# Performance work log

Measured on AMD Instinct MI355X. Metric: run time of the kernel, lower is better.

Reference implementation:

```python
import jax, jax.numpy as jnp
import numpy as np

EMBED_DIM = 2048
NUM_HEADS = 16
HEAD_DIM = EMBED_DIM // NUM_HEADS
ROPE_BASE = 10000.0


def _rope_cos_sin(seq_len, head_dim, dtype):
    # half-split (LLaMA-style) rotary embedding tables, shape [S, D]
    inv_freq = 1.0 / (ROPE_BASE ** (jnp.arange(0, head_dim, 2, dtype=jnp.float32) / head_dim))
    ang = jnp.arange(seq_len, dtype=jnp.float32)[:, None] * inv_freq[None, :]  # [S, D/2]
    cos = jnp.concatenate([jnp.cos(ang), jnp.cos(ang)], axis=-1).astype(dtype)
    sin = jnp.concatenate([jnp.sin(ang), jnp.sin(ang)], axis=-1).astype(dtype)
    return cos, sin


def _rotate_half(t):
    d = t.shape[-1] // 2
    return jnp.concatenate([-t[..., d:], t[..., :d]], axis=-1)


def setup_inputs() -> dict:
    key = jax.random.key(0)
    ks = jax.random.split(key, 9)
    B, S, E = 2, 2048, EMBED_DIM
    sc = 1.0 / np.sqrt(E)
    return {
        "x": jax.random.normal(ks[0], (B, S, E), jnp.float32),
        "Wq": jax.random.normal(ks[1], (E, E), jnp.float32) * sc,
        "bq": jax.random.normal(ks[2], (E,), jnp.float32) * 0.01,
        "Wk": jax.random.normal(ks[3], (E, E), jnp.float32) * sc,
        "bk": jax.random.normal(ks[4], (E,), jnp.float32) * 0.01,
        "Wv": jax.random.normal(ks[5], (E, E), jnp.float32) * sc,
        "bv": jax.random.normal(ks[6], (E,), jnp.float32) * 0.01,
        "Wo": jax.random.normal(ks[7], (E, E), jnp.float32) * sc,
        "bo": jax.random.normal(ks[8], (E,), jnp.float32) * 0.01,
    }


def reference(x, Wq, bq, Wk, bk, Wv, bv, Wo, bo):
    B, S, E = x.shape
    H, D = NUM_HEADS, HEAD_DIM

    def split_heads(t):  # [B,S,E] -> [B,H,S,D]
        return t.reshape(B, S, H, D).transpose(0, 2, 1, 3)

    # torch nn.Linear: y = x @ W^T + b
    q = split_heads(x @ Wq.T + bq)
    k = split_heads(x @ Wk.T + bk)
    v = split_heads(x @ Wv.T + bv)

    cos, sin = _rope_cos_sin(S, D, x.dtype)  # [S, D]
    q = q * cos + _rotate_half(q) * sin
    k = k * cos + _rotate_half(k) * sin

    scale = 1.0 / jnp.sqrt(jnp.asarray(D, x.dtype))
    scores = jnp.einsum("bhsd,bhtd->bhst", q, k) * scale  # [B,H,S,S]
    attn = jax.nn.softmax(scores, axis=-1)
    ctx = jnp.einsum("bhst,bhtd->bhsd", attn, v)  # [B,H,S,D]
    ctx = ctx.transpose(0, 2, 1, 3).reshape(B, S, E)
    return ctx @ Wo.T + bo
```

## Files before the change

kernel.cpp:

```cpp
#include <hip/hip_runtime.h>
#include <stdint.h>

typedef unsigned short u16;
typedef unsigned int u32;
typedef __bf16 bf16x8 __attribute__((ext_vector_type(8)));
typedef u16 u16x8 __attribute__((ext_vector_type(8)));
typedef float f32x4 __attribute__((ext_vector_type(4)));
typedef float f32x16 __attribute__((ext_vector_type(16)));

#define NB 2
#define NS 2048
#define NE 2048
#define NH 16
#define ND 128
#define NM (NB*NS)

__device__ __forceinline__ float bf2f(u16 u){
  union { unsigned u; float f; } v; v.u = ((unsigned)u) << 16; return v.f;
}
__device__ __forceinline__ u16 f2bf(float f){
  union { float f; unsigned u; } v; v.f = f;
  unsigned r = v.u + 0x7fffu + ((v.u >> 16) & 1u);
  return (u16)(r >> 16);
}
__device__ __forceinline__ void gl_lds16(const u16* g, u16* l){
  __builtin_amdgcn_global_load_lds((const __attribute__((address_space(1))) unsigned int*)g,
                                   (__attribute__((address_space(3))) unsigned int*)l, 16, 0, 0);
}

__global__ __launch_bounds__(256) void k_prep(const float* __restrict__ x,
                                              const float* __restrict__ w0, const float* __restrict__ w1,
                                              const float* __restrict__ w2, const float* __restrict__ w3,
                                              u16* __restrict__ xo,
                                              u16* __restrict__ o0, u16* __restrict__ o1,
                                              u16* __restrict__ o2, u16* __restrict__ o3,
                                              float* __restrict__ cosT, float* __restrict__ sinT){
  const int NX = NM * NE / 4;
  const int NW = NE * NE / 4;
  const int NC = NX + 4 * NW;
  const int NT = NS * 64;
  const int TOT = NC + NT;
  for (int i = blockIdx.x * 256 + threadIdx.x; i < TOT; i += gridDim.x * 256){
    if (i < NC){
      const float* in; u16* out; int off;
      if (i < NX){ in = x; out = xo; off = i; }
      else {
        int j = i - NX; int sg = j >> 20; off = j & (NW - 1);
        in  = sg == 0 ? w0 : sg == 1 ? w1 : sg == 2 ? w2 : w3;
        out = sg == 0 ? o0 : sg == 1 ? o1 : sg == 2 ? o2 : o3;
      }
      float4 v = ((const float4*)in)[off];
      ushort4 o;
      o.x = f2bf(v.x); o.y = f2bf(v.y); o.z = f2bf(v.z); o.w = f2bf(v.w);
      ((ushort4*)out)[off] = o;
    } else {
      int idx = i - NC;
      int s = idx >> 6, ii = idx & 63;
      float inv = exp2f(-(float)(2 * ii) * (13.287712379549449f / 128.0f));
      float ang = (float)s * inv;
      float c = cosf(ang), sn = sinf(ang);
      cosT[s * ND + ii]      = c;  cosT[s * ND + 64 + ii] = c;
      sinT[s * ND + ii]      = sn; sinT[s * ND + 64 + ii] = sn;
    }
  }
}

template<int MODE>
__global__ __launch_bounds__(512, 2) void k_gemm(const u16* __restrict__ A, const u16* __restrict__ W,
                                                 const float* __restrict__ bias,
                                                 const float* __restrict__ cosT, const float* __restrict__ sinT,
                                                 float qs, void* __restrict__ outp)
{
  __shared__ __align__(16) u16 lds[49152];
  const int t    = threadIdx.x;
  const int lane = t & 63;
  const int g    = lane >> 4;
  const int q    = lane & 15;
  const int wid  = t >> 6;
  const int wr   = (wid >> 1) * 64;
  const int wc   = (wid & 1) * 64;

  const int bid = blockIdx.x;
  const int v   = (bid & 7) * 32 + (bid >> 3);
  const int bm  = (v >> 4) * 256;
  const int bn  = (v & 15) * 128;

  int aoff[4], aldso[4], boff[2], bldso[2];
  #pragma unroll
  for (int c = 0; c < 4; ++c){
    int o = c * 8192 + t * 16;
    int row = o >> 7;
    int cb = (o & 127) ^ ((row & 7) << 4);
    aldso[c] = o >> 1;
    aoff[c]  = row * NE + (cb >> 1);
  }
  #pragma unroll
  for (int c = 0; c < 2; ++c){
    int o = c * 8192 + t * 16;
    int row = o >> 7;
    int cb = (o & 127) ^ ((row & 7) << 4);
    bldso[c] = o >> 1;
    boff[c]  = row * NE + (cb >> 1);
  }
  const u16* Abase = A + (size_t)bm * NE;
  const u16* Wbase = W + (size_t)bn * NE;

  int ard[2][4], brd[2][4];
  #pragma unroll
  for (int kk = 0; kk < 2; ++kk){
    #pragma unroll
    for (int m = 0; m < 4; ++m){
      int row = wr + m * 16 + q;
      ard[kk][m] = row * 128 + ((kk * 64 + g * 16) ^ ((row & 7) << 4));
    }
    #pragma unroll
    for (int n = 0; n < 4; ++n){
      int row = wc + n * 16 + q;
      brd[kk][n] = row * 128 + ((kk * 64 + g * 16) ^ ((row & 7) << 4));
    }
  }

  #pragma unroll
  for (int c = 0; c < 4; ++c) gl_lds16(Abase + aoff[c], lds + aldso[c]);
  #pragma unroll
  for (int c = 0; c < 2; ++c) gl_lds16(Wbase + boff[c], lds + 16384 + bldso[c]);

  f32x4 acc[4][4] = {};

  for (int kt = 0; kt < 32; ++kt){
    const int cbb = (kt & 1) ? 24576 : 0;
    if (kt < 31){
      const int sbb = cbb ^ 24576;
      const int go  = (kt + 1) * 64;
      #pragma unroll
      for (int c = 0; c < 4; ++c) gl_lds16(Abase + go + aoff[c], lds + sbb + aldso[c]);
      #pragma unroll
      for (int c = 0; c < 2; ++c) gl_lds16(Wbase + go + boff[c], lds + sbb + 16384 + bldso[c]);
      asm volatile("s_waitcnt vmcnt(6)" ::: "memory");
    } else {
      asm volatile("s_waitcnt vmcnt(0)" ::: "memory");
    }
    __builtin_amdgcn_s_barrier();

    const char* Ap = (const char*)(lds + cbb);
    const char* Bp = (const char*)(lds + cbb + 16384);

    #pragma unroll
    for (int kk = 0; kk < 2; ++kk){
      bf16x8 af[4], bfr[4];
      #pragma unroll
      for (int m = 0; m < 4; ++m) af[m]  = *(const bf16x8*)(Ap + ard[kk][m]);
      #pragma unroll
      for (int n = 0; n < 4; ++n) bfr[n] = *(const bf16x8*)(Bp + brd[kk][n]);
      __builtin_amdgcn_s_setprio(1);
      #pragma unroll
      for (int m = 0; m < 4; ++m)
        #pragma unroll
        for (int n = 0; n < 4; ++n)
          acc[m][n] = __builtin_amdgcn_mfma_f32_16x16x32_bf16(af[m], bfr[n], acc[m][n], 0, 0, 0);
      __builtin_amdgcn_s_setprio(0);
    }
    __builtin_amdgcn_s_barrier();
  }

  if constexpr (MODE == 2){
    float* out = (float*)outp;
    #pragma unroll
    for (int m = 0; m < 4; ++m)
      #pragma unroll
      for (int n = 0; n < 4; ++n){
        int col = bn + wc + n * 16 + q;
        float bv = bias[col];
        #pragma unroll
        for (int j = 0; j < 4; ++j){
          int row = bm + wr + m * 16 + g * 4 + j;
          out[(size_t)row * NE + col] = acc[m][n][j] + bv;
        }
      }
  } else if constexpr (MODE == 1){
    u16* out = (u16*)outp;
    __syncthreads();
    #pragma unroll
    for (int m = 0; m < 4; ++m)
      #pragma unroll
      for (int n = 0; n < 4; ++n){
        int d = wc + n * 16 + q;
        float bv = bias[bn + d];
        #pragma unroll
        for (int j = 0; j < 4; ++j){
          int sl = wr + m * 16 + g * 4 + j;
          lds[d * 264 + sl] = f2bf(acc[m][n][j] + bv);
        }
      }
    __syncthreads();
    const int b = bm >> 11, h = bn >> 7, sbase = bm & 2047;
    const int dq = t >> 4;
    const int sq = (t & 15) * 16;
    #pragma unroll
    for (int rep = 0; rep < 4; ++rep){
      int d = rep * 32 + dq;
      const u16* src = lds + d * 264 + sq;
      u16* dp = out + ((size_t)((b * NH + h) * ND + d)) * NS + sbase + sq;
      *(u16x8*)(dp)     = *(const u16x8*)(src);
      *(u16x8*)(dp + 8) = *(const u16x8*)(src + 8);
    }
  } else {
    u16* out = (u16*)outp;
    __syncthreads();
    #pragma unroll
    for (int m = 0; m < 4; ++m)
      #pragma unroll
      for (int n = 0; n < 4; ++n){
        int cl = wc + n * 16 + q;
        float bv = bias[bn + cl];
        #pragma unroll
        for (int j = 0; j < 4; ++j){
          int rl = wr + m * 16 + g * 4 + j;
          lds[rl * 132 + cl] = f2bf(acc[m][n][j] + bv);
        }
      }
    __syncthreads();
    #pragma unroll
    for (int m = 0; m < 4; ++m)
      #pragma unroll
      for (int n = 0; n < 4; ++n){
        int cl  = wc + n * 16 + q;
        int col = bn + cl;
        int h = col >> 7;
        float bv = bias[col];
        #pragma unroll
        for (int j = 0; j < 4; ++j){
          int rl = wr + m * 16 + g * 4 + j;
          int row = bm + rl;
          int b = row >> 11, s = row & 2047;
          float mine    = acc[m][n][j] + bv;
          float partner = bf2f(lds[rl * 132 + (cl ^ 64)]);
          float rot = (cl < 64) ? -partner : partner;
          float val = (mine * cosT[s * ND + cl] + rot * sinT[s * ND + cl]) * qs;
          out[(((size_t)(b * NH + h)) * NS + s) * ND + cl] = f2bf(val);
        }
      }
  }
}

template<bool D1>
__device__ __forceinline__ void pswap(u32 &a, u32 &b){
  if constexpr (D1) asm volatile("v_permlane32_swap_b32 %0, %1" : "+v"(a), "+v"(b));
  else              asm volatile("v_permlane32_swap_b32 %0, %1" : "+v"(b), "+v"(a));
}

#define AT_BODY(KT, SCC, SCN, KSTG, VSTG, KNXT, VCUR, SK, SV, VM, LAST)               \
  {                                                                                   \
    if (SK){ const int kb = ((KT) + 2) * 64 * ND;                                     \
      _Pragma("unroll") for (int c = 0; c < 4; ++c)                                   \
        gl_lds16(Kbase + kb + koff[c], (KSTG) + kldso[c]); }                          \
    if (SV){ const int vb = ((KT) + 1) * 64;                                          \
      _Pragma("unroll") for (int c = 0; c < 4; ++c)                                   \
        gl_lds16(Vbase + vb + voff[c], (VSTG) + vldso[c]); }                          \
    asm volatile("s_waitcnt vmcnt(" VM ")" ::: "memory");                             \
    __builtin_amdgcn_s_barrier();                                                     \
    float ts = 0.f;                                                                   \
    if (!(LAST)){                                                                     \
      SCN[0] = (f32x16)(0.f);                                                         \
      __builtin_amdgcn_s_setprio(1);                                                  \
      _Pragma("unroll") for (int kk = 0; kk < 8; ++kk){                               \
        bf16x8 kf = *(const bf16x8*)((KNXT) + krd[0][kk]);                            \
        SCN[0] = __builtin_amdgcn_mfma_f32_32x32x16_bf16(kf, qf[kk], SCN[0], 0, 0, 0);\
      }                                                                               \
      __builtin_amdgcn_s_setprio(0);                                                  \
    }                                                                                 \
    _Pragma("unroll") for (int r = 0; r < 16; ++r){                                   \
      float e = exp2f(SCC[0][r]); SCC[0][r] = e; ts += e; }                           \
    if (!(LAST)){                                                                     \
      SCN[1] = (f32x16)(0.f);                                                         \
      __builtin_amdgcn_s_setprio(1);                                                  \
      _Pragma("unroll") for (int kk = 0; kk < 8; ++kk){                               \
        bf16x8 kf = *(const bf16x8*)((KNXT) + krd[1][kk]);                            \
        SCN[1] = __builtin_amdgcn_mfma_f32_32x32x16_bf16(kf, qf[kk], SCN[1], 0, 0, 0);\
      }                                                                               \
      __builtin_amdgcn_s_setprio(0);                                                  \
    }                                                                                 \
    _Pragma("unroll") for (int r = 0; r < 16; ++r){                                   \
      float e = exp2f(SCC[1][r]); SCC[1][r] = e; ts += e; }                           \
    ts += __shfl_xor(ts, 32);                                                         \
    lrow += ts;                                                                       \
    __builtin_amdgcn_s_setprio(1);                                                    \
    _Pragma("unroll") for (int t2 = 0; t2 < 2; ++t2)                                  \
      _Pragma("unroll") for (int kk2 = 0; kk2 < 2; ++kk2){                            \
        u32 a0, a1, b0, b1;                                                           \
        asm("v_cvt_pk_bf16_f32 %0, %1, %2" : "=v"(a0) : "v"(SCC[t2][8*kk2+0]), "v"(SCC[t2][8*kk2+1])); \
        asm("v_cvt_pk_bf16_f32 %0, %1, %2" : "=v"(a1) : "v"(SCC[t2][8*kk2+2]), "v"(SCC[t2][8*kk2+3])); \
        asm("v_cvt_pk_bf16_f32 %0, %1, %2" : "=v"(b0) : "v"(SCC[t2][8*kk2+4]), "v"(SCC[t2][8*kk2+5])); \
        asm("v_cvt_pk_bf16_f32 %0, %1, %2" : "=v"(b1) : "v"(SCC[t2][8*kk2+6]), "v"(SCC[t2][8*kk2+7])); \
        pswap<D1>(a0, b0); pswap<D1>(a1, b1);                                         \
        union { u32 u[4]; bf16x8 v; } pf;                                             \
        pf.u[0] = a0; pf.u[1] = a1; pf.u[2] = b0; pf.u[3] = b1;                       \
        const int kkf = 2*t2 + kk2;                                                   \
        _Pragma("unroll") for (int dt = 0; dt < 4; ++dt){                             \
          bf16x8 vf = *(const bf16x8*)((VCUR) + vrd[kkf][dt]);                        \
          acc[dt] = __builtin_amdgcn_mfma_f32_32x32x16_bf16(vf, pf.v, acc[dt], 0, 0, 0); \
        }                                                                             \
      }                                                                               \
    __builtin_amdgcn_s_setprio(0);                                                    \
    if (!(LAST)) __builtin_amdgcn_s_barrier();                                        \
  }

template<bool D1>
__device__ __forceinline__ void attn_impl(const u16* __restrict__ Qa, const u16* __restrict__ Ka,
                                          const u16* __restrict__ Vt, u16* __restrict__ ctx,
                                          u16* Ks0, u16* Ks1, u16* Vs0, u16* Vs1)
{
  const int t    = threadIdx.x;
  const int lane = t & 63;
  const int w    = t >> 6;
  const int l31  = lane & 31;
  const int hi   = lane >> 5;

  const int v   = (blockIdx.x & 7) * 64 + (blockIdx.x >> 3);
  const int qb  = v & 15;
  const int bh  = v >> 4;
  const int q0  = qb * 128 + w * 32;

  int koff[4], kldso[4], voff[4], vldso[4];
  #pragma unroll
  for (int c = 0; c < 4; ++c){
    int o = c * 4096 + t * 16;
    { int row = o >> 8, col = o & 255; int cs = col ^ ((row & 15) << 4);
      kldso[c] = o >> 1;  koff[c] = row * ND + (cs >> 1); }
    { int row = o >> 7, col = o & 127; int cs = col ^ ((row & 7) << 4);
      vldso[c] = o >> 1;  voff[c] = row * NS + (cs >> 1); }
  }
  const u16* Kbase = Ka + (size_t)bh * NS * ND;
  const u16* Vbase = Vt + (size_t)bh * ND * NS;

  bf16x8 qf[8];
  #pragma unroll
  for (int kk = 0; kk < 8; ++kk)
    qf[kk] = *(const bf16x8*)(Qa + ((size_t)bh * NS + q0 + l31) * ND + kk * 16 + hi * 8);

  #pragma unroll
  for (int c = 0; c < 4; ++c) gl_lds16(Kbase + koff[c], Ks0 + kldso[c]);
  #pragma unroll
  for (int c = 0; c < 4; ++c) gl_lds16(Vbase + voff[c], Vs0 + vldso[c]);
  #pragma unroll
  for (int c = 0; c < 4; ++c) gl_lds16(Kbase + 64 * ND + koff[c], Ks1 + kldso[c]);

  int krd[2][8], vrd[4][4];
  #pragma unroll
  for (int t2 = 0; t2 < 2; ++t2){
    const int row = t2 * 32 + l31, sw = (row & 15) << 4;
    #pragma unroll
    for (int kk = 0; kk < 8; ++kk)
      krd[t2][kk] = row * 256 + ((kk * 32 + hi * 16) ^ sw);
  }
  #pragma unroll
  for (int dt = 0; dt < 4; ++dt){
    const int row = dt * 32 + l31, sw = (row & 7) << 4;
    #pragma unroll
    for (int kk = 0; kk < 4; ++kk)
      vrd[kk][dt] = row * 128 + ((kk * 32 + hi * 16) ^ sw);
  }

  asm volatile("s_waitcnt vmcnt(8)" ::: "memory");
  __builtin_amdgcn_s_barrier();

  f32x16 scA[2], scB[2];
  scA[0] = (f32x16)(0.f); scA[1] = (f32x16)(0.f);
  {
    const char* Kl = (const char*)Ks0;
    #pragma unroll
    for (int t2 = 0; t2 < 2; ++t2)
      #pragma unroll
      for (int kk = 0; kk < 8; ++kk){
        bf16x8 kf = *(const bf16x8*)(Kl + krd[t2][kk]);
        scA[t2] = __builtin_amdgcn_mfma_f32_32x32x16_bf16(kf, qf[kk], scA[t2], 0, 0, 0);
      }
  }
  __builtin_amdgcn_s_barrier();

  f32x16 acc[4] = {};
  float lrow = 0.f;

  for (int kt = 0; kt < 30; kt += 2){
    AT_BODY(kt,     scA, scB, Ks0, Vs1, (const char*)Ks1, (const char*)Vs0, 1, 1, "8", 0);
    AT_BODY(kt + 1, scB, scA, Ks1, Vs0, (const char*)Ks0, (const char*)Vs1, 1, 1, "8", 0);
  }
  AT_BODY(30, scA, scB, Ks0, Vs1, (const char*)Ks1, (const char*)Vs0, 0, 1, "4", 0);
  AT_BODY(31, scB, scA, Ks1, Vs0, (const char*)Ks0, (const char*)Vs1, 0, 0, "0", 1);

  const float inv = 1.0f / lrow;
  const int b = bh >> 4, h = bh & 15;
  const int s = q0 + l31;
  #pragma unroll
  for (int dt = 0; dt < 4; ++dt)
    #pragma unroll
    for (int a2 = 0; a2 < 4; ++a2){
      const int d0 = dt * 32 + 8 * a2 + 4 * hi;
      ushort4 o;
      o.x = f2bf(acc[dt][4*a2+0] * inv);
      o.y = f2bf(acc[dt][4*a2+1] * inv);
      o.z = f2bf(acc[dt][4*a2+2] * inv);
      o.w = f2bf(acc[dt][4*a2+3] * inv);
      *(ushort4*)(ctx + ((size_t)(b * NS + s)) * NE + h * ND + d0) = o;
    }
}

__global__ __launch_bounds__(256, 2) void k_attn(const u16* __restrict__ Qa, const u16* __restrict__ Ka,
                                                 const u16* __restrict__ Vt, u16* __restrict__ ctx)
{
  __shared__ __align__(16) u16 Ks[2][64 * 128];
  __shared__ __align__(16) u16 Vs[2][128 * 64];
  const int lane = threadIdx.x & 63;
  u32 xx = (u32)lane, yy = 64u + (u32)lane;
  asm volatile("v_permlane32_swap_b32 %0, %1" : "+v"(xx), "+v"(yy));
  const bool isD1 = (xx == (u32)(lane < 32 ? lane : lane + 32));
  if (isD1) attn_impl<true >(Qa, Ka, Vt, ctx, &Ks[0][0], &Ks[1][0], &Vs[0][0], &Vs[1][0]);
  else      attn_impl<false>(Qa, Ka, Vt, ctx, &Ks[0][0], &Ks[1][0], &Vs[0][0], &Vs[1][0]);
}

extern "C" void kernel_launch(void* const* d_in, const int* in_sizes, int n_in,
                              void* d_out, int out_size, void* d_ws, size_t ws_size,
                              hipStream_t stream)
{
  const float* x  = (const float*)d_in[0];
  const float* Wq = (const float*)d_in[1];
  const float* bq = (const float*)d_in[2];
  const float* Wk = (const float*)d_in[3];
  const float* bk = (const float*)d_in[4];
  const float* Wv = (const float*)d_in[5];
  const float* bv = (const float*)d_in[6];
  const float* Wo = (const float*)d_in[7];
  const float* bo = (const float*)d_in[8];

  char* ws = (char*)d_ws;
  u16*   xbf  = (u16*)(ws);
  u16*   wqb  = (u16*)(ws + 16777216);
  u16*   wkb  = (u16*)(ws + 25165824);
  u16*   wvb  = (u16*)(ws + 33554432);
  u16*   wob  = (u16*)(ws + 41943040);
  float* cosT = (float*)(ws + 50331648);
  float* sinT = (float*)(ws + 51380224);
  u16*   Qa   = (u16*)(ws + 52428800);
  u16*   Ka   = (u16*)(ws + 69206016);
  u16*   Vt   = (u16*)(ws + 85983232);
  u16*   ctx  = xbf;

  const float sl = 0.08838834764831845f * 1.4426950408889634f;

  k_prep<<<2048, 256, 0, stream>>>(x, Wq, Wk, Wv, Wo, xbf, wqb, wkb, wvb, wob, cosT, sinT);

  k_gemm<0><<<256, 512, 0, stream>>>(xbf, wqb, bq, cosT, sinT, sl,   (void*)Qa);
  k_gemm<0><<<256, 512, 0, stream>>>(xbf, wkb, bk, cosT, sinT, 1.0f, (void*)Ka);
  k_gemm<1><<<256, 512, 0, stream>>>(xbf, wvb, bv, nullptr, nullptr, 1.0f, (void*)Vt);

  k_attn<<<512, 256, 0, stream>>>(Qa, Ka, Vt, ctx);

  k_gemm<2><<<256, 512, 0, stream>>>(ctx, wob, bo, nullptr, nullptr, 1.0f, d_out);
}
```

Measured before the change: 269.7 us.

## Fuse Q/K/V projections into one GEMM launch with triple-buffered LDS

Replaces the three separate Q, K and V projection GEMM launches with one 768-block kernel over a concatenated weight (wqb, wkb, wvb assumed contiguous), picking the epilogue per column segment. The K-loop moves from double to triple buffering of LDS (73728 u16 = 144 KB), which drops the trailing barrier per iteration. The attention row-sum cross-lane shuffle is hoisted out of the inner loop to a single final shuffle. Risks: 144 KB LDS per block limits residency to one block per CU despite launch_bounds(512,2), and removing the end-of-iteration barrier relies on the third buffer to avoid overwrite races.

```diff
diff --git a/kernel.cpp b/kernel.cpp
--- a/kernel.cpp
+++ b/kernel.cpp
@@ -65,154 +65,133 @@
   }
 }
 
-template<int MODE>
-__global__ __launch_bounds__(512, 2) void k_gemm(const u16* __restrict__ A, const u16* __restrict__ W,
-                                                 const float* __restrict__ bias,
-                                                 const float* __restrict__ cosT, const float* __restrict__ sinT,
-                                                 float qs, void* __restrict__ outp)
+#define GEMM_PREAMBLE                                                                 \
+  const int t    = threadIdx.x;                                                      \
+  const int lane = t & 63;                                                           \
+  const int g    = lane >> 4;                                                        \
+  const int q    = lane & 15;                                                        \
+  const int wid  = t >> 6;                                                           \
+  const int wr   = (wid >> 1) * 64;                                                  \
+  const int wc   = (wid & 1) * 64;                                                   \
+  int aoff[4], aldso[4], boff[2], bldso[2];                                          \
+  _Pragma("unroll") for (int c = 0; c < 4; ++c){                                     \
+    int o = c * 8192 + t * 16;                                                       \
+    int row = o >> 7;                                                                \
+    int cb2 = (o & 127) ^ ((row & 7) << 4);                                          \
+    aldso[c] = o >> 1;                                                               \
+    aoff[c]  = row * NE + (cb2 >> 1);                                                \
+  }                                                                                  \
+  _Pragma("unroll") for (int c = 0; c < 2; ++c){                                     \
+    int o = c * 8192 + t * 16;                                                       \
+    int row = o >> 7;                                                                \
+    int cb2 = (o & 127) ^ ((row & 7) << 4);                                          \
+    bldso[c] = o >> 1;                                                               \
+    boff[c]  = row * NE + (cb2 >> 1);                                                \
+  }                                                                                  \
+  int ard[2][4], brd[2][4];                                                          \
+  _Pragma("unroll") for (int kk = 0; kk < 2; ++kk){                                  \
+    _Pragma("unroll") for (int m = 0; m < 4; ++m){                                   \
+      int row = wr + m * 16 + q;                                                     \
+      ard[kk][m] = row * 128 + ((kk * 64 + g * 16) ^ ((row & 7) << 4));              \
+    }                                                                                \
+    _Pragma("unroll") for (int n = 0; n < 4; ++n){                                   \
+      int row = wc + n * 16 + q;                                                     \
+      brd[kk][n] = row * 128 + ((kk * 64 + g * 16) ^ ((row & 7) << 4));              \
+    }                                                                                \
+  }
+
+#define GEMM_KLOOP(Abase, Wbase, lds)                                                \
+  _Pragma("unroll") for (int c = 0; c < 4; ++c) gl_lds16((Abase) + aoff[c], (lds) + aldso[c]); \
+  _Pragma("unroll") for (int c = 0; c < 2; ++c) gl_lds16((Wbase) + boff[c], (lds) + 16384 + bldso[c]); \
+  f32x4 acc[4][4] = {};                                                              \
+  int cbb = 0, sbb = 24576;                                                          \
+  for (int kt = 0; kt < 32; ++kt){                                                   \
+    if (kt < 31){                                                                    \
+      const int go = (kt + 1) * 64;                                                  \
+      _Pragma("unroll") for (int c = 0; c < 4; ++c) gl_lds16((Abase) + go + aoff[c], (lds) + sbb + aldso[c]); \
+      _Pragma("unroll") for (int c = 0; c < 2; ++c) gl_lds16((Wbase) + go + boff[c], (lds) + sbb + 16384 + bldso[c]); \
+      asm volatile("s_waitcnt vmcnt(6)" ::: "memory");                               \
+    } else {                                                                         \
+      asm volatile("s_waitcnt vmcnt(0)" ::: "memory");                               \
+    }                                                                                \
+    __builtin_amdgcn_s_barrier();                                                    \
+    const char* Ap = (const char*)((lds) + cbb);                                     \
+    const char* Bp = (const char*)((lds) + cbb + 16384);                             \
+    _Pragma("unroll") for (int kk = 0; kk < 2; ++kk){                                \
+      bf16x8 af[4], bfr[4];                                                          \
+      _Pragma("unroll") for (int m = 0; m < 4; ++m) af[m]  = *(const bf16x8*)(Ap + ard[kk][m]); \
+      _Pragma("unroll") for (int n = 0; n < 4; ++n) bfr[n] = *(const bf16x8*)(Bp + brd[kk][n]); \
+      __builtin_amdgcn_s_setprio(1);                                                 \
+      _Pragma("unroll") for (int m = 0; m < 4; ++m)                                  \
+        _Pragma("unroll") for (int n = 0; n < 4; ++n)                                \
+          acc[m][n] = __builtin_amdgcn_mfma_f32_16x16x32_bf16(af[m], bfr[n], acc[m][n], 0, 0, 0); \
+      __builtin_amdgcn_s_setprio(0);                                                 \
+    }                                                                                \
+    cbb = (cbb == 49152) ? 0 : cbb + 24576;                                          \
+    sbb = (sbb == 49152) ? 0 : sbb + 24576;                                          \
+  }
+
+__global__ __launch_bounds__(512, 2) void k_gemm_qkv(const u16* __restrict__ A, const u16* __restrict__ Wqkv,
+                                                     const float* __restrict__ bq, const float* __restrict__ bk,
+                                                     const float* __restrict__ bvv,
+                                                     const float* __restrict__ cosT, const float* __restrict__ sinT,
+                                                     float sl, u16* __restrict__ Qa, u16* __restrict__ Ka,
+                                                     u16* __restrict__ Vt)
 {
-  __shared__ __align__(16) u16 lds[49152];
-  const int t    = threadIdx.x;
-  const int lane = t & 63;
-  const int g    = lane >> 4;
-  const int q    = lane & 15;
-  const int wid  = t >> 6;
-  const int wr   = (wid >> 1) * 64;
-  const int wc   = (wid & 1) * 64;
-
+  __shared__ __align__(16) u16 lds[73728];
+  GEMM_PREAMBLE
   const int bid = blockIdx.x;
-  const int v   = (bid & 7) * 32 + (bid >> 3);
-  const int bm  = (v >> 4) * 256;
-  const int bn  = (v & 15) * 128;
-
-  int aoff[4], aldso[4], boff[2], bldso[2];
-  #pragma unroll
-  for (int c = 0; c < 4; ++c){
-    int o = c * 8192 + t * 16;
-    int row = o >> 7;
-    int cb = (o & 127) ^ ((row & 7) << 4);
-    aldso[c] = o >> 1;
-    aoff[c]  = row * NE + (cb >> 1);
-  }
-  #pragma unroll
-  for (int c = 0; c < 2; ++c){
-    int o = c * 8192 + t * 16;
-    int row = o >> 7;
-    int cb = (o & 127) ^ ((row & 7) << 4);
-    bldso[c] = o >> 1;
-    boff[c]  = row * NE + (cb >> 1);
-  }
-  const u16* Abase = A + (size_t)bm * NE;
-  const u16* Wbase = W + (size_t)bn * NE;
-
-  int ard[2][4], brd[2][4];
-  #pragma unroll
-  for (int kk = 0; kk < 2; ++kk){
-    #pragma unroll
-    for (int m = 0; m < 4; ++m){
-      int row = wr + m * 16 + q;
-      ard[kk][m] = row * 128 + ((kk * 64 + g * 16) ^ ((row & 7) << 4));
-    }
-    #pragma unroll
-    for (int n = 0; n < 4; ++n){
-      int row = wc + n * 16 + q;
-      brd[kk][n] = row * 128 + ((kk * 64 + g * 16) ^ ((row & 7) << 4));
-    }
-  }
-
-  #pragma unroll
-  for (int c = 0; c < 4; ++c) gl_lds16(Abase + aoff[c], lds + aldso[c]);
-  #pragma unroll
-  for (int c = 0; c < 2; ++c) gl_lds16(Wbase + boff[c], lds + 16384 + bldso[c]);
-
-  f32x4 acc[4][4] = {};
-
-  for (int kt = 0; kt < 32; ++kt){
-    const int cbb = (kt & 1) ? 24576 : 0;
-    if (kt < 31){
-      const int sbb = cbb ^ 24576;
-      const int go  = (kt + 1) * 64;
-      #pragma unroll
-      for (int c = 0; c < 4; ++c) gl_lds16(Abase + go + aoff[c], lds + sbb + aldso[c]);
-      #pragma unroll
-      for (int c = 0; c < 2; ++c) gl_lds16(Wbase + go + boff[c], lds + sbb + 16384 + bldso[c]);
-      asm volatile("s_waitcnt vmcnt(6)" ::: "memory");
-    } else {
-      asm volatile("s_waitcnt vmcnt(0)" ::: "memory");
-    }
-    __builtin_amdgcn_s_barrier();
-
-    const char* Ap = (const char*)(lds + cbb);
-    const char* Bp = (const char*)(lds + cbb + 16384);
-
-    #pragma unroll
-    for (int kk = 0; kk < 2; ++kk){
-      bf16x8 af[4], bfr[4];
-      #pragma unroll
-      for (int m = 0; m < 4; ++m) af[m]  = *(const bf16x8*)(Ap + ard[kk][m]);
-      #pragma unroll
-      for (int n = 0; n < 4; ++n) bfr[n] = *(const bf16x8*)(Bp + brd[kk][n]);
-      __builtin_amdgcn_s_setprio(1);
-      #pragma unroll
-      for (int m = 0; m < 4; ++m)
-        #pragma unroll
-        for (int n = 0; n < 4; ++n)
-          acc[m][n] = __builtin_amdgcn_mfma_f32_16x16x32_bf16(af[m], bfr[n], acc[m][n], 0, 0, 0);
-      __builtin_amdgcn_s_setprio(0);
-    }
-    __builtin_amdgcn_s_barrier();
-  }
-
-  if constexpr (MODE == 2){
-    float* out = (float*)outp;
-    #pragma unroll
-    for (int m = 0; m < 4; ++m)
-      #pragma unroll
-      for (int n = 0; n < 4; ++n){
-        int col = bn + wc + n * 16 + q;
-        float bv = bias[col];
-        #pragma unroll
-        for (int j = 0; j < 4; ++j){
-          int row = bm + wr + m * 16 + g * 4 + j;
-          out[(size_t)row * NE + col] = acc[m][n][j] + bv;
-        }
-      }
-  } else if constexpr (MODE == 1){
-    u16* out = (u16*)outp;
+  const int v   = (bid & 7) * 96 + (bid >> 3);
+  const int mi  = v / 48;
+  const int ni  = v - mi * 48;
+  const int bm  = mi * 256;
+  const int bn  = ni * 128;
+
+  const u16* Abase = A    + (size_t)bm * NE;
+  const u16* Wbase = Wqkv + (size_t)bn * NE;
+
+  GEMM_KLOOP(Abase, Wbase, lds)
+
+  const int seg = bn >> 11;
+  const int bnn = bn & 2047;
+  if (seg == 2){
+    const float* bias = bvv;
     __syncthreads();
     #pragma unroll
     for (int m = 0; m < 4; ++m)
       #pragma unroll
       for (int n = 0; n < 4; ++n){
         int d = wc + n * 16 + q;
-        float bv = bias[bn + d];
+        float bv = bias[bnn + d];
         #pragma unroll
         for (int j = 0; j < 4; ++j){
-          int sl = wr + m * 16 + g * 4 + j;
-          lds[d * 264 + sl] = f2bf(acc[m][n][j] + bv);
+          int sl2 = wr + m * 16 + g * 4 + j;
+          lds[d * 264 + sl2] = f2bf(acc[m][n][j] + bv);
         }
       }
     __syncthreads();
-    const int b = bm >> 11, h = bn >> 7, sbase = bm & 2047;
+    const int b = bm >> 11, h = bnn >> 7, sbase = bm & 2047;
     const int dq = t >> 4;
     const int sq = (t & 15) * 16;
     #pragma unroll
     for (int rep = 0; rep < 4; ++rep){
       int d = rep * 32 + dq;
       const u16* src = lds + d * 264 + sq;
-      u16* dp = out + ((size_t)((b * NH + h) * ND + d)) * NS + sbase + sq;
+      u16* dp = Vt + ((size_t)((b * NH + h) * ND + d)) * NS + sbase + sq;
       *(u16x8*)(dp)     = *(const u16x8*)(src);
       *(u16x8*)(dp + 8) = *(const u16x8*)(src + 8);
     }
   } else {
-    u16* out = (u16*)outp;
+    const float* bias = seg ? bk : bq;
+    const float  qs   = seg ? 1.0f : sl;
+    u16* out = seg ? Ka : Qa;
     __syncthreads();
     #pragma unroll
     for (int m = 0; m < 4; ++m)
       #pragma unroll
       for (int n = 0; n < 4; ++n){
         int cl = wc + n * 16 + q;
-        float bv = bias[bn + cl];
+        float bv = bias[bnn + cl];
         #pragma unroll
         for (int j = 0; j < 4; ++j){
           int rl = wr + m * 16 + g * 4 + j;
@@ -225,7 +204,7 @@
       #pragma unroll
       for (int n = 0; n < 4; ++n){
         int cl  = wc + n * 16 + q;
-        int col = bn + cl;
+        int col = bnn + cl;
         int h = col >> 7;
         float bv = bias[col];
         #pragma unroll
@@ -241,6 +220,35 @@
         }
       }
   }
+}
+
+__global__ __launch_bounds__(512, 2) void k_gemm_o(const u16* __restrict__ A, const u16* __restrict__ W,
+                                                   const float* __restrict__ bias, float* __restrict__ out)
+{
+  __shared__ __align__(16) u16 lds[73728];
+  GEMM_PREAMBLE
+  const int bid = blockIdx.x;
+  const int v   = (bid & 7) * 32 + (bid >> 3);
+  const int bm  = (v >> 4) * 256;
+  const int bn  = (v & 15) * 128;
+
+  const u16* Abase = A + (size_t)bm * NE;
+  const u16* Wbase = W + (size_t)bn * NE;
+
+  GEMM_KLOOP(Abase, Wbase, lds)
+
+  #pragma unroll
+  for (int m = 0; m < 4; ++m)
+    #pragma unroll
+    for (int n = 0; n < 4; ++n){
+      int col = bn + wc + n * 16 + q;
+      float bv = bias[col];
+      #pragma unroll
+      for (int j = 0; j < 4; ++j){
+        int row = bm + wr + m * 16 + g * 4 + j;
+        out[(size_t)row * NE + col] = acc[m][n][j] + bv;
+      }
+    }
 }
 
 template<bool D1>
@@ -282,7 +290,6 @@
     }                                                                                 \
     _Pragma("unroll") for (int r = 0; r < 16; ++r){                                   \
       float e = exp2f(SCC[1][r]); SCC[1][r] = e; ts += e; }                           \
-    ts += __shfl_xor(ts, 32);                                                         \
     lrow += ts;                                                                       \
     __builtin_amdgcn_s_setprio(1);                                                    \
     _Pragma("unroll") for (int t2 = 0; t2 < 2; ++t2)                                  \
@@ -388,6 +395,7 @@
   AT_BODY(30, scA, scB, Ks0, Vs1, (const char*)Ks1, (const char*)Vs0, 0, 1, "4", 0);
   AT_BODY(31, scB, scA, Ks1, Vs0, (const char*)Ks0, (const char*)Vs1, 0, 0, "0", 1);
 
+  lrow += __shfl_xor(lrow, 32);
   const float inv = 1.0f / lrow;
   const int b = bh >> 4, h = bh & 15;
   const int s = q0 + l31;
@@ -449,11 +457,9 @@
 
   k_prep<<<2048, 256, 0, stream>>>(x, Wq, Wk, Wv, Wo, xbf, wqb, wkb, wvb, wob, cosT, sinT);
 
-  k_gemm<0><<<256, 512, 0, stream>>>(xbf, wqb, bq, cosT, sinT, sl,   (void*)Qa);
-  k_gemm<0><<<256, 512, 0, stream>>>(xbf, wkb, bk, cosT, sinT, 1.0f, (void*)Ka);
-  k_gemm<1><<<256, 512, 0, stream>>>(xbf, wvb, bv, nullptr, nullptr, 1.0f, (void*)Vt);
+  k_gemm_qkv<<<768, 512, 0, stream>>>(xbf, wqb, bq, bk, bv, cosT, sinT, sl, Qa, Ka, Vt);
 
   k_attn<<<512, 256, 0, stream>>>(Qa, Ka, Vt, ctx);
 
-  k_gemm<2><<<256, 512, 0, stream>>>(ctx, wob, bo, nullptr, nullptr, 1.0f, d_out);
-}
+  k_gemm_o<<<256, 512, 0, stream>>>(ctx, wob, bo, (float*)d_out);
+}
```

New measurement: 253.8 us. -5.9%, faster.

## Fuse Q/K/V projections into one 256x256-tile GEMM and triple-buffer output GEMM

Applied to the files above, without the earlier changes.

Replaces three separate QKV projection launches with a single GEMM over concatenated weights (wqb/wkb/wvb assumed contiguous). It uses 256x256 tiles on 384 blocks and routes each tile's epilogue to RoPE+Q scaling, K RoPE, or V transpose by column segment. The output projection becomes a dedicated kernel with a three-stage LDS ring that drops the trailing barrier per k-step. The attention kernel also moves a cross-lane row-sum shuffle out of the inner loop to the end. Larger tiles raise register and LDS use and force one block per CU for the QKV GEMM.

```diff
diff --git a/kernel.cpp b/kernel.cpp
--- a/kernel.cpp
+++ b/kernel.cpp
@@ -65,13 +65,176 @@
   }
 }
 
-template<int MODE>
-__global__ __launch_bounds__(512, 2) void k_gemm(const u16* __restrict__ A, const u16* __restrict__ W,
-                                                 const float* __restrict__ bias,
-                                                 const float* __restrict__ cosT, const float* __restrict__ sinT,
-                                                 float qs, void* __restrict__ outp)
+__global__ __launch_bounds__(512, 1) void k_gemm_qkv(const u16* __restrict__ A, const u16* __restrict__ Wqkv,
+                                                     const float* __restrict__ bq, const float* __restrict__ bk,
+                                                     const float* __restrict__ bvv,
+                                                     const float* __restrict__ cosT, const float* __restrict__ sinT,
+                                                     float sl, u16* __restrict__ Qa, u16* __restrict__ Ka,
+                                                     u16* __restrict__ Vt)
 {
-  __shared__ __align__(16) u16 lds[49152];
+  __shared__ __align__(16) u16 lds[67584];
+  const int t    = threadIdx.x;
+  const int lane = t & 63;
+  const int g    = lane >> 4;
+  const int q    = lane & 15;
+  const int w    = t >> 6;
+  const int wr   = (w >> 2) * 128;
+  const int wc   = (w & 3) * 64;
+
+  const int bid = blockIdx.x;
+  const int v   = (bid & 7) * 48 + (bid >> 3);
+  const int mi  = v / 24;
+  const int ni  = v - mi * 24;
+  const int bm  = mi * 256;
+  const int bn  = ni * 256;
+
+  int soff[4], sldo[4];
+  #pragma unroll
+  for (int c = 0; c < 4; ++c){
+    int o = c * 8192 + t * 16;
+    int row = o >> 7;
+    int cb = (o & 127) ^ ((row & 7) << 4);
+    sldo[c] = o >> 1;
+    soff[c] = row * NE + (cb >> 1);
+  }
+  const u16* Abase = A    + (size_t)bm * NE;
+  const u16* Wbase = Wqkv + (size_t)bn * NE;
+
+  int ard[2][8], brd[2][4];
+  #pragma unroll
+  for (int kk = 0; kk < 2; ++kk){
+    #pragma unroll
+    for (int m = 0; m < 8; ++m){
+      int row = wr + m * 16 + q;
+      ard[kk][m] = row * 128 + ((kk * 64 + g * 16) ^ ((row & 7) << 4));
+    }
+    #pragma unroll
+    for (int n = 0; n < 4; ++n){
+      int row = wc + n * 16 + q;
+      brd[kk][n] = row * 128 + ((kk * 64 + g * 16) ^ ((row & 7) << 4));
+    }
+  }
+
+  #pragma unroll
+  for (int c = 0; c < 4; ++c) gl_lds16(Abase + soff[c], lds + sldo[c]);
+  #pragma unroll
+  for (int c = 0; c < 4; ++c) gl_lds16(Wbase + soff[c], lds + 16384 + sldo[c]);
+
+  f32x4 acc[8][4] = {};
+
+  for (int kt = 0; kt < 32; ++kt){
+    const int cbb = (kt & 1) ? 32768 : 0;
+    if (kt < 31){
+      const int sbb = cbb ^ 32768;
+      const int go  = (kt + 1) * 64;
+      #pragma unroll
+      for (int c = 0; c < 4; ++c) gl_lds16(Abase + go + soff[c], lds + sbb + sldo[c]);
+      #pragma unroll
+      for (int c = 0; c < 4; ++c) gl_lds16(Wbase + go + soff[c], lds + sbb + 16384 + sldo[c]);
+      asm volatile("s_waitcnt vmcnt(8)" ::: "memory");
+    } else {
+      asm volatile("s_waitcnt vmcnt(0)" ::: "memory");
+    }
+    __builtin_amdgcn_s_barrier();
+
+    const char* Ap = (const char*)(lds + cbb);
+    const char* Bp = Ap + 32768;
+
+    #pragma unroll
+    for (int kk = 0; kk < 2; ++kk){
+      bf16x8 af[8], bfr[4];
+      #pragma unroll
+      for (int m = 0; m < 8; ++m) af[m]  = *(const bf16x8*)(Ap + ard[kk][m]);
+      #pragma unroll
+      for (int n = 0; n < 4; ++n) bfr[n] = *(const bf16x8*)(Bp + brd[kk][n]);
+      __builtin_amdgcn_s_setprio(1);
+      #pragma unroll
+      for (int m = 0; m < 8; ++m)
+        #pragma unroll
+        for (int n = 0; n < 4; ++n)
+          acc[m][n] = __builtin_amdgcn_mfma_f32_16x16x32_bf16(af[m], bfr[n], acc[m][n], 0, 0, 0);
+      __builtin_amdgcn_s_setprio(0);
+    }
+    __builtin_amdgcn_s_barrier();
+  }
+
+  const int seg = ni >> 3;
+  const int bnn = (ni & 7) * 256;
+  const int b   = bm >> 11;
+  const int sbase = bm & 2047;
+
+  if (seg == 2){
+    __syncthreads();
+    #pragma unroll
+    for (int m = 0; m < 8; ++m)
+      #pragma unroll
+      for (int n = 0; n < 4; ++n){
+        int cl = wc + n * 16 + q;
+        float bv = bvv[bnn + cl];
+        #pragma unroll
+        for (int j = 0; j < 4; ++j){
+          int sl2 = wr + m * 16 + g * 4 + j;
+          lds[cl * 264 + sl2] = f2bf(acc[m][n][j] + bv);
+        }
+      }
+    __syncthreads();
+    const int h0 = bnn >> 7;
+    const int dq = t >> 4;
+    const int sq = (t & 15) * 16;
+    #pragma unroll
+    for (int rep = 0; rep < 8; ++rep){
+      int dd = rep * 32 + dq;
+      int hh = dd >> 7, d = dd & 127;
+      const u16* src = lds + dd * 264 + sq;
+      u16* dp = Vt + ((size_t)((b * NH + h0 + hh) * ND + d)) * NS + sbase + sq;
+      *(u16x8*)(dp)     = *(const u16x8*)(src);
+      *(u16x8*)(dp + 8) = *(const u16x8*)(src + 8);
+    }
+  } else {
+    const float* bias = seg ? bk : bq;
+    const float  qs   = seg ? 1.0f : sl;
+    u16* out = seg ? Ka : Qa;
+    __syncthreads();
+    #pragma unroll
+    for (int m = 0; m < 8; ++m)
+      #pragma unroll
+      for (int n = 0; n < 4; ++n){
+        int cl = wc + n * 16 + q;
+        float bv = bias[bnn + cl];
+        #pragma unroll
+        for (int j = 0; j < 4; ++j){
+          int rl = wr + m * 16 + g * 4 + j;
+          lds[rl * 264 + cl] = f2bf(acc[m][n][j] + bv);
+        }
+      }
+    __syncthreads();
+    #pragma unroll
+    for (int m = 0; m < 8; ++m)
+      #pragma unroll
+      for (int n = 0; n < 4; ++n){
+        int cl  = wc + n * 16 + q;
+        int col = bnn + cl;
+        int h  = col >> 7;
+        int dd = col & 127;
+        float bv = bias[col];
+        #pragma unroll
+        for (int j = 0; j < 4; ++j){
+          int rl = wr + m * 16 + g * 4 + j;
+          int s = sbase + rl;
+          float mine    = acc[m][n][j] + bv;
+          float partner = bf2f(lds[rl * 264 + (cl ^ 64)]);
+          float rot = (dd < 64) ? -partner : partner;
+          float val = (mine * cosT[s * ND + dd] + rot * sinT[s * ND + dd]) * qs;
+          out[(((size_t)(b * NH + h)) * NS + s) * ND + dd] = f2bf(val);
+        }
+      }
+  }
+}
+
+__global__ __launch_bounds__(512, 2) void k_gemm_o(const u16* __restrict__ A, const u16* __restrict__ W,
+                                                   const float* __restrict__ bias, float* __restrict__ out)
+{
+  __shared__ __align__(16) u16 lds[73728];
   const int t    = threadIdx.x;
   const int lane = t & 63;
   const int g    = lane >> 4;
@@ -79,7 +242,6 @@
   const int wid  = t >> 6;
   const int wr   = (wid >> 1) * 64;
   const int wc   = (wid & 1) * 64;
-
   const int bid = blockIdx.x;
   const int v   = (bid & 7) * 32 + (bid >> 3);
   const int bm  = (v >> 4) * 256;
@@ -90,17 +252,17 @@
   for (int c = 0; c < 4; ++c){
     int o = c * 8192 + t * 16;
     int row = o >> 7;
-    int cb = (o & 127) ^ ((row & 7) << 4);
+    int cb2 = (o & 127) ^ ((row & 7) << 4);
     aldso[c] = o >> 1;
-    aoff[c]  = row * NE + (cb >> 1);
+    aoff[c]  = row * NE + (cb2 >> 1);
   }
   #pragma unroll
   for (int c = 0; c < 2; ++c){
     int o = c * 8192 + t * 16;
     int row = o >> 7;
-    int cb = (o & 127) ^ ((row & 7) << 4);
+    int cb2 = (o & 127) ^ ((row & 7) << 4);
     bldso[c] = o >> 1;
-    boff[c]  = row * NE + (cb >> 1);
+    boff[c]  = row * NE + (cb2 >> 1);
   }
   const u16* Abase = A + (size_t)bm * NE;
   const u16* Wbase = W + (size_t)bn * NE;
@@ -126,12 +288,10 @@
   for (int c = 0; c < 2; ++c) gl_lds16(Wbase + boff[c], lds + 16384 + bldso[c]);
 
   f32x4 acc[4][4] = {};
-
+  int cbb = 0, sbb = 24576;
   for (int kt = 0; kt < 32; ++kt){
-    const int cbb = (kt & 1) ? 24576 : 0;
     if (kt < 31){
-      const int sbb = cbb ^ 24576;
-      const int go  = (kt + 1) * 64;
+      const int go = (kt + 1) * 64;
       #pragma unroll
       for (int c = 0; c < 4; ++c) gl_lds16(Abase + go + aoff[c], lds + sbb + aldso[c]);
       #pragma unroll
@@ -141,10 +301,8 @@
       asm volatile("s_waitcnt vmcnt(0)" ::: "memory");
     }
     __builtin_amdgcn_s_barrier();
-
     const char* Ap = (const char*)(lds + cbb);
     const char* Bp = (const char*)(lds + cbb + 16384);
-
     #pragma unroll
     for (int kk = 0; kk < 2; ++kk){
       bf16x8 af[4], bfr[4];
@@ -160,87 +318,22 @@
           acc[m][n] = __builtin_amdgcn_mfma_f32_16x16x32_bf16(af[m], bfr[n], acc[m][n], 0, 0, 0);
       __builtin_amdgcn_s_setprio(0);
     }
-    __builtin_amdgcn_s_barrier();
-  }
-
-  if constexpr (MODE == 2){
-    float* out = (float*)outp;
-    #pragma unroll
-    for (int m = 0; m < 4; ++m)
-      #pragma unroll
-      for (int n = 0; n < 4; ++n){
-        int col = bn + wc + n * 16 + q;
-        float bv = bias[col];
-        #pragma unroll
-        for (int j = 0; j < 4; ++j){
-          int row = bm + wr + m * 16 + g * 4 + j;
-          out[(size_t)row * NE + col] = acc[m][n][j] + bv;
-        }
+    cbb = (cbb == 49152) ? 0 : cbb + 24576;
+    sbb = (sbb == 49152) ? 0 : sbb + 24576;
+  }
+
+  #pragma unroll
+  for (int m = 0; m < 4; ++m)
+    #pragma unroll
+    for (int n = 0; n < 4; ++n){
+      int col = bn + wc + n * 16 + q;
+      float bv = bias[col];
+      #pragma unroll
+      for (int j = 0; j < 4; ++j){
+        int row = bm + wr + m * 16 + g * 4 + j;
+        out[(size_t)row * NE + col] = acc[m][n][j] + bv;
       }
-  } else if constexpr (MODE == 1){
-    u16* out = (u16*)outp;
-    __syncthreads();
-    #pragma unroll
-    for (int m = 0; m < 4; ++m)
-      #pragma unroll
-      for (int n = 0; n < 4; ++n){
-        int d = wc + n * 16 + q;
-        float bv = bias[bn + d];
-        #pragma unroll
-        for (int j = 0; j < 4; ++j){
-          int sl = wr + m * 16 + g * 4 + j;
-          lds[d * 264 + sl] = f2bf(acc[m][n][j] + bv);
-        }
-      }
-    __syncthreads();
-    const int b = bm >> 11, h = bn >> 7, sbase = bm & 2047;
-    const int dq = t >> 4;
-    const int sq = (t & 15) * 16;
-    #pragma unroll
-    for (int rep = 0; rep < 4; ++rep){
-      int d = rep * 32 + dq;
-      const u16* src = lds + d * 264 + sq;
-      u16* dp = out + ((size_t)((b * NH + h) * ND + d)) * NS + sbase + sq;
-      *(u16x8*)(dp)     = *(const u16x8*)(src);
-      *(u16x8*)(dp + 8) = *(const u16x8*)(src + 8);
-    }
-  } else {
-    u16* out = (u16*)outp;
-    __syncthreads();
-    #pragma unroll
-    for (int m = 0; m < 4; ++m)
-      #pragma unroll
-      for (int n = 0; n < 4; ++n){
-        int cl = wc + n * 16 + q;
-        float bv = bias[bn + cl];
-        #pragma unroll
-        for (int j = 0; j < 4; ++j){
-          int rl = wr + m * 16 + g * 4 + j;
-          lds[rl * 132 + cl] = f2bf(acc[m][n][j] + bv);
-        }
-      }
-    __syncthreads();
-    #pragma unroll
-    for (int m = 0; m < 4; ++m)
-      #pragma unroll
-      for (int n = 0; n < 4; ++n){
-        int cl  = wc + n * 16 + q;
-        int col = bn + cl;
-        int h = col >> 7;
-        float bv = bias[col];
-        #pragma unroll
-        for (int j = 0; j < 4; ++j){
-          int rl = wr + m * 16 + g * 4 + j;
-          int row = bm + rl;
-          int b = row >> 11, s = row & 2047;
-          float mine    = acc[m][n][j] + bv;
-          float partner = bf2f(lds[rl * 132 + (cl ^ 64)]);
-          float rot = (cl < 64) ? -partner : partner;
-          float val = (mine * cosT[s * ND + cl] + rot * sinT[s * ND + cl]) * qs;
-          out[(((size_t)(b * NH + h)) * NS + s) * ND + cl] = f2bf(val);
-        }
-      }
-  }
+    }
 }
 
 template<bool D1>
@@ -282,7 +375,6 @@
     }                                                                                 \
     _Pragma("unroll") for (int r = 0; r < 16; ++r){                                   \
       float e = exp2f(SCC[1][r]); SCC[1][r] = e; ts += e; }                           \
-    ts += __shfl_xor(ts, 32);                                                         \
     lrow += ts;                                                                       \
     __builtin_amdgcn_s_setprio(1);                                                    \
     _Pragma("unroll") for (int t2 = 0; t2 < 2; ++t2)                                  \
@@ -388,6 +480,7 @@
   AT_BODY(30, scA, scB, Ks0, Vs1, (const char*)Ks1, (const char*)Vs0, 0, 1, "4", 0);
   AT_BODY(31, scB, scA, Ks1, Vs0, (const char*)Ks0, (const char*)Vs1, 0, 0, "0", 1);
 
+  lrow += __shfl_xor(lrow, 32);
   const float inv = 1.0f / lrow;
   const int b = bh >> 4, h = bh & 15;
   const int s = q0 + l31;
@@ -449,11 +542,9 @@
 
   k_prep<<<2048, 256, 0, stream>>>(x, Wq, Wk, Wv, Wo, xbf, wqb, wkb, wvb, wob, cosT, sinT);
 
-  k_gemm<0><<<256, 512, 0, stream>>>(xbf, wqb, bq, cosT, sinT, sl,   (void*)Qa);
-  k_gemm<0><<<256, 512, 0, stream>>>(xbf, wkb, bk, cosT, sinT, 1.0f, (void*)Ka);
-  k_gemm<1><<<256, 512, 0, stream>>>(xbf, wvb, bv, nullptr, nullptr, 1.0f, (void*)Vt);
+  k_gemm_qkv<<<384, 512, 0, stream>>>(xbf, wqb, bq, bk, bv, cosT, sinT, sl, Qa, Ka, Vt);
 
   k_attn<<<512, 256, 0, stream>>>(Qa, Ka, Vt, ctx);
 
-  k_gemm<2><<<256, 512, 0, stream>>>(ctx, wob, bo, nullptr, nullptr, 1.0f, d_out);
-}
+  k_gemm_o<<<256, 512, 0, stream>>>(ctx, wob, bo, (float*)d_out);
+}
```

Measured after the change: 269.1 us. No clear change (-0.2%).
